# Optimization experiments

Hardware: AMD Instinct MI355X
Metric: run time of the kernel (lower is better)

## Reference

```python
import jax, jax.numpy as jnp
import numpy as np

WINDOW = (7, 7)
SHIFT = (3, 3)
NUM_HEADS = 8
MASK_VALUE = -100.0


def _relative_position_index(wh, ww):
    ch, cw = np.arange(wh), np.arange(ww)
    coords = np.stack(np.meshgrid(ch, cw, indexing='ij'))          # (2, wh, ww)
    cf = coords.reshape(2, -1)                                      # (2, N)
    rel = (cf[:, :, None] - cf[:, None, :]).transpose(1, 2, 0)      # (N, N, 2)
    rel[..., 0] += wh - 1
    rel[..., 1] += ww - 1
    rel[..., 0] *= 2 * ww - 1
    return rel.sum(-1)                                              # (N, N)


def _shift_attn_mask(pH, pW, wh, ww, sh, sw):
    # region-id image for the cyclic shift, as in torchvision Swin
    img = np.zeros((pH, pW), dtype=np.float32)
    cnt = 0
    for hs in ((0, -wh), (-wh, -sh), (-sh, None)):
        for ws_ in ((0, -ww), (-ww, -sw), (-sw, None)):
            img[hs[0]:hs[1], ws_[0]:ws_[1]] = cnt
            cnt += 1
    mw = img.reshape(pH // wh, wh, pW // ww, ww).transpose(0, 2, 1, 3).reshape(-1, wh * ww)
    diff = mw[:, None, :] - mw[:, :, None]                          # (nWtot, N, N)
    return np.where(diff != 0, MASK_VALUE, 0.0).astype(np.float32)


def setup_inputs() -> dict:
    key = jax.random.key(0)
    ks = jax.random.split(key, 6)
    B, H, W, C = 32, 56, 56, 256
    return {
        'x': jax.random.normal(ks[0], (B, H, W, C), jnp.float32),
        'qkv_w': jax.random.normal(ks[1], (3 * C, C), jnp.float32) * 0.02,
        'qkv_b': jax.random.normal(ks[2], (3 * C,), jnp.float32) * 0.02,
        'proj_w': jax.random.normal(ks[3], (C, C), jnp.float32) * 0.02,
        'proj_b': jax.random.normal(ks[4], (C,), jnp.float32) * 0.02,
        'rel_bias_table': jax.random.normal(ks[5], ((2 * WINDOW[0] - 1) * (2 * WINDOW[1] - 1), NUM_HEADS), jnp.float32) * 0.02,
    }


def reference(x, qkv_w, qkv_b, proj_w, proj_b, rel_bias_table):
    wh, ww = WINDOW
    B, H, W, C = x.shape
    nh = NUM_HEADS
    hd = C // nh
    N = wh * ww

    # pad right/bottom to window multiples (static)
    pad_r = (ww - W % ww) % ww
    pad_b = (wh - H % wh) % wh
    x = jnp.pad(x, ((0, 0), (0, pad_b), (0, pad_r), (0, 0)))
    pH, pW = H + pad_b, W + pad_r

    sh = 0 if wh >= pH else SHIFT[0]
    sw = 0 if ww >= pW else SHIFT[1]
    shifted = (sh + sw) > 0
    if shifted:
        x = jnp.roll(x, shift=(-sh, -sw), axis=(1, 2))

    nH, nW = pH // wh, pW // ww
    nwin = nH * nW
    # window partition -> (B*nwin, N, C)
    xw = x.reshape(B, nH, wh, nW, ww, C).transpose(0, 1, 3, 2, 4, 5).reshape(B * nwin, N, C)

    # qkv projection (torch Linear: x @ W.T + b)
    qkv = jnp.einsum('bnc,oc->bno', xw, qkv_w) + qkv_b
    qkv = qkv.reshape(B * nwin, N, 3, nh, hd).transpose(2, 0, 3, 1, 4)  # (3, Bn, h, N, hd)
    q, k, v = qkv[0], qkv[1], qkv[2]

    q = q * (hd ** -0.5)
    attn = jnp.einsum('bhnd,bhmd->bhnm', q, k)                      # (Bn, h, N, N)

    # relative position bias
    idx = jnp.asarray(_relative_position_index(wh, ww))             # (N, N)
    bias = rel_bias_table[idx.reshape(-1)].reshape(N, N, nh).transpose(2, 0, 1)
    attn = attn + bias[None]

    if shifted:
        amask = jnp.asarray(_shift_attn_mask(pH, pW, wh, ww, sh, sw))  # (nwin, N, N)
        attn = attn.reshape(B, nwin, nh, N, N) + amask[None, :, None]
        attn = attn.reshape(B * nwin, nh, N, N)

    attn = jax.nn.softmax(attn, axis=-1)
    out = jnp.einsum('bhnm,bhmd->bhnd', attn, v)                    # (Bn, h, N, hd)
    out = out.transpose(0, 2, 1, 3).reshape(B * nwin, N, C)
    out = jnp.einsum('bnc,oc->bno', out, proj_w) + proj_b

    # window reverse
    out = out.reshape(B, nH, nW, wh, ww, C).transpose(0, 1, 3, 2, 4, 5).reshape(B, pH, pW, C)
    if shifted:
        out = jnp.roll(out, shift=(sh, sw), axis=(1, 2))
    return out[:, :H, :W, :]
```

## Files before the change

kernel.cpp:

```cpp
#include <hip/hip_runtime.h>

typedef __attribute__((ext_vector_type(8))) short bf16x8;
typedef __attribute__((ext_vector_type(4))) float f32x4;
typedef unsigned short u16;

#define NTOK    49
#define SCALE   0.17677669529663687f
#define NEGBIG  -30000.0f
#define DIV7(v) (((v) * 9363) >> 16)

#define EX_OFF     0
#define EX_BYTES   28704
#define EX_INIT_B  25872
#define XO_OFF     28704
#define XO_BYTES   25872
#define BIAS_OFF   54576
#define BIAS_BYTES 2704
#define SMEM_BYTES 57280

static __device__ __forceinline__ float b2f(u16 u) {
    return __uint_as_float(((unsigned int)u) << 16);
}
static __device__ __forceinline__ u16 f2b(float f) {
    unsigned int x = __float_as_uint(f);
    x += 0x7fffu + ((x >> 16) & 1u);
    return (u16)(x >> 16);
}
static __device__ __forceinline__ bf16x8 load8(const void* base, int eidx, int isbf) {
    if (isbf) return *(const bf16x8*)((const u16*)base + eidx);
    const float* f = (const float*)base + eidx;
    float4 a = *(const float4*)f;
    float4 c = *(const float4*)(f + 4);
    bf16x8 r;
    r[0] = (short)f2b(a.x); r[1] = (short)f2b(a.y); r[2] = (short)f2b(a.z); r[3] = (short)f2b(a.w);
    r[4] = (short)f2b(c.x); r[5] = (short)f2b(c.y); r[6] = (short)f2b(c.z); r[7] = (short)f2b(c.w);
    return r;
}
static __device__ __forceinline__ float loadf(const void* base, int i, int isbf) {
    return isbf ? b2f(((const u16*)base)[i]) : ((const float*)base)[i];
}
static __device__ __forceinline__ int region9(int gh, int gw) {
    return (gh < 49 ? 0 : (gh < 53 ? 1 : 2)) * 3 + (gw < 49 ? 0 : (gw < 53 ? 1 : 2));
}

__global__ void __launch_bounds__(256, 2)
swin_fused_v5(const void* __restrict__ x, const void* __restrict__ qkv_w,
              const void* __restrict__ qkv_b, const void* __restrict__ proj_w,
              const void* __restrict__ proj_b, const void* __restrict__ bias_tbl,
              void* __restrict__ out)
{
    __shared__ __align__(16) char smem[SMEM_BYTES];
    const int tid    = threadIdx.x;
    const int wv     = tid >> 6;
    const int lane   = tid & 63;
    const int lane15 = lane & 15;
    const int quad   = lane >> 4;
    const int crow   = quad << 2;

    const int win  = blockIdx.x;
    const int b    = win >> 6;
    const int wrem = win & 63;
    const int whi  = wrem >> 3;
    const int wwi  = wrem & 7;

    int good = 0;
#pragma unroll
    for (int j = 0; j < 8; ++j) {
        u16 u = ((const u16*)qkv_w)[lane * 32 + j * 4];
        int e = (u >> 7) & 0xff;
        good += (e == 0 || (e >= 100 && e <= 140)) ? 1 : 0;
    }
#pragma unroll
    for (int d = 1; d < 64; d <<= 1) good += __shfl_xor(good, d, 64);
    const int isbf = (good > 300) ? 1 : 0;

    for (int i = tid; i < NTOK * 32; i += 256) {
        int tok = i >> 5, ch = i & 31;
        int rt = DIV7(tok), ct = tok - rt * 7;
        int sh_ = whi * 7 + rt + 3; if (sh_ >= 56) sh_ -= 56;
        int sw_ = wwi * 7 + ct + 3; if (sw_ >= 56) sw_ -= 56;
        int idx = ((b * 56 + sh_) * 56 + sw_) * 256 + ch * 8;
        *(bf16x8*)(smem + XO_OFF + tok * 528 + ch * 16) = load8(x, idx, isbf);
    }
    for (int i = tid; i < 169 * 8; i += 256)
        *(u16*)(smem + BIAS_OFF + i * 2) = f2b(loadf(bias_tbl, i, isbf));
    {
        bf16x8 z8 = {0, 0, 0, 0, 0, 0, 0, 0};
        for (int i = tid; i < (EX_BYTES - EX_INIT_B) / 16; i += 256)
            *(bf16x8*)(smem + EX_OFF + EX_INIT_B + i * 16) = z8;
        for (int r = tid; r < NTOK; r += 256)
            *(bf16x8*)(smem + EX_OFF + r * 528 + 512) = z8;
    }
    __syncthreads();

    int mrowc[4];
#pragma unroll
    for (int t = 0; t < 4; ++t) {
        int m = t * 16 + lane15;
        mrowc[t] = m < 49 ? m : 48;
    }

    bf16x8 fragQ[2][4], fragK[2][4], fragV[2][4];

#pragma unroll
    for (int rnd = 0; rnd < 2; ++rnd) {
        for (int ci = 0; ci < 4; ++ci) {
            int o = (wv * 4 + ci) * 16 + lane15;
            int orow = rnd * 256 + o;
            f32x4 acc[4];
#pragma unroll
            for (int t = 0; t < 4; ++t) acc[t] = (f32x4){0.f, 0.f, 0.f, 0.f};
#pragma unroll
            for (int ks = 0; ks < 8; ++ks) {
                bf16x8 bfrag = load8(qkv_w, orow * 256 + ks * 32 + quad * 8, isbf);
                int cb = (ks * 32 + quad * 8) * 2;
#pragma unroll
                for (int tm = 0; tm < 4; ++tm) {
                    bf16x8 afrag = *(const bf16x8*)(smem + XO_OFF + mrowc[tm] * 528 + cb);
                    acc[tm] = __builtin_amdgcn_mfma_f32_16x16x32_bf16(afrag, bfrag, acc[tm], 0, 0, 0);
                }
            }
            float bias = loadf(qkv_b, orow, isbf);
#pragma unroll
            for (int tm = 0; tm < 4; ++tm)
#pragma unroll
                for (int rr = 0; rr < 4; ++rr) {
                    int row = tm * 16 + crow + rr;
                    if (row < 49)
                        *(u16*)(smem + EX_OFF + (row * 264 + o) * 2) = f2b(acc[tm][rr] + bias);
                }
        }
        __syncthreads();
#pragma unroll
        for (int hi = 0; hi < 2; ++hi)
#pragma unroll
            for (int t = 0; t < 4; ++t) {
                bf16x8 f = *(const bf16x8*)(smem + EX_OFF +
                            (mrowc[t] * 264 + wv * 64 + hi * 32 + quad * 8) * 2);
                if (rnd == 0) fragQ[hi][t] = f; else fragK[hi][t] = f;
            }
        __syncthreads();
    }

    for (int ci = 0; ci < 4; ++ci) {
        int vch = (wv * 4 + ci) * 16 + lane15;
        int orow = 512 + vch;
        f32x4 acc[4];
#pragma unroll
        for (int t = 0; t < 4; ++t) acc[t] = (f32x4){0.f, 0.f, 0.f, 0.f};
#pragma unroll
        for (int ks = 0; ks < 8; ++ks) {
            bf16x8 bfrag = load8(qkv_w, orow * 256 + ks * 32 + quad * 8, isbf);
            int cb = (ks * 32 + quad * 8) * 2;
#pragma unroll
            for (int tm = 0; tm < 4; ++tm) {
                bf16x8 afrag = *(const bf16x8*)(smem + XO_OFF + mrowc[tm] * 528 + cb);
                acc[tm] = __builtin_amdgcn_mfma_f32_16x16x32_bf16(afrag, bfrag, acc[tm], 0, 0, 0);
            }
        }
        float bias = loadf(qkv_b, orow, isbf);
#pragma unroll
        for (int tm = 0; tm < 4; ++tm)
#pragma unroll
            for (int rr = 0; rr < 4; ++rr) {
                int row = tm * 16 + crow + rr;
                if (row < 49)
                    *(u16*)(smem + EX_OFF + (vch * 56 + row) * 2) = f2b(acc[tm][rr] + bias);
            }
    }
    __syncthreads();
#pragma unroll
    for (int hi = 0; hi < 2; ++hi)
#pragma unroll
        for (int f = 0; f < 4; ++f) {
            int vrow = wv * 64 + hi * 32 + (f & 1) * 16 + lane15;
            int vcol = (f >> 1) * 32 + quad * 8;
            fragV[hi][f] = *(const bf16x8*)(smem + EX_OFF + (vrow * 56 + vcol) * 2);
        }
    __syncthreads();

    int nval[4], regn_[4], idxn[4];
#pragma unroll
    for (int tn = 0; tn < 4; ++tn) {
        int n = tn * 16 + lane15;
        nval[tn] = (n < 49);
        int nc = n < 49 ? n : 48;
        int rn = DIV7(nc), cn = nc - rn * 7;
        regn_[tn] = region9(whi * 7 + rn, wwi * 7 + cn);
        idxn[tn]  = (6 - rn) * 13 + (6 - cn);
    }

    char* pbase = smem + EX_OFF + wv * 7056;
#pragma unroll
    for (int hi = 0; hi < 2; ++hi) {
        int h = wv * 2 + hi;
        f32x4 s[4][4];
#pragma unroll
        for (int tm = 0; tm < 4; ++tm)
#pragma unroll
            for (int tn = 0; tn < 4; ++tn) {
                f32x4 z = {0.f, 0.f, 0.f, 0.f};
                s[tm][tn] = __builtin_amdgcn_mfma_f32_16x16x32_bf16(fragQ[hi][tm], fragK[hi][tn], z, 0, 0, 0);
            }
#pragma unroll
        for (int tm = 0; tm < 4; ++tm)
#pragma unroll
            for (int rr = 0; rr < 4; ++rr) {
                int m = tm * 16 + crow + rr;
                int mc2 = m < 49 ? m : 48;
                int rm = DIV7(mc2), cm = mc2 - rm * 7;
                int regm = region9(whi * 7 + rm, wwi * 7 + cm);
                int basem = rm * 13 + cm;
                float e[4];
                float mv = NEGBIG;
#pragma unroll
                for (int tn = 0; tn < 4; ++tn) {
                    float v;
                    if (nval[tn]) {
                        int idx = basem + idxn[tn];
                        float bv = b2f(*(const u16*)(smem + BIAS_OFF + (idx * 8 + h) * 2));
                        v = s[tm][tn][rr] * SCALE + bv + ((regm != regn_[tn]) ? -100.0f : 0.0f);
                    } else v = NEGBIG;
                    e[tn] = v;
                    mv = fmaxf(mv, v);
                }
#pragma unroll
                for (int d = 1; d < 16; d <<= 1) mv = fmaxf(mv, __shfl_xor(mv, d, 16));
                float ssum = 0.f;
#pragma unroll
                for (int tn = 0; tn < 4; ++tn) {
                    e[tn] = __expf(e[tn] - mv);
                    ssum += e[tn];
                }
#pragma unroll
                for (int d = 1; d < 16; d <<= 1) ssum += __shfl_xor(ssum, d, 16);
                float ri = 1.0f / ssum;
                if (m < 49) {
#pragma unroll
                    for (int tn = 0; tn < 4; ++tn) {
                        int n = tn * 16 + lane15;
                        u16 hv = nval[tn] ? f2b(e[tn] * ri) : (u16)0;
                        *(u16*)(pbase + (m * 72 + n) * 2) = hv;
                    }
                }
            }
        __syncthreads();
        f32x4 ov0[4], ov1[4];
#pragma unroll
        for (int tm = 0; tm < 4; ++tm) {
            ov0[tm] = (f32x4){0.f, 0.f, 0.f, 0.f};
            ov1[tm] = (f32x4){0.f, 0.f, 0.f, 0.f};
        }
#pragma unroll
        for (int ks = 0; ks < 2; ++ks) {
            int kb = (ks * 32 + quad * 8) * 2;
#pragma unroll
            for (int tm = 0; tm < 4; ++tm) {
                bf16x8 ap = *(const bf16x8*)(pbase + mrowc[tm] * 144 + kb);
                ov0[tm] = __builtin_amdgcn_mfma_f32_16x16x32_bf16(ap, fragV[hi][ks * 2],     ov0[tm], 0, 0, 0);
                ov1[tm] = __builtin_amdgcn_mfma_f32_16x16x32_bf16(ap, fragV[hi][ks * 2 + 1], ov1[tm], 0, 0, 0);
            }
        }
#pragma unroll
        for (int tm = 0; tm < 4; ++tm)
#pragma unroll
            for (int rr = 0; rr < 4; ++rr) {
                int row = tm * 16 + crow + rr;
                if (row < 49) {
                    *(u16*)(smem + XO_OFF + (row * 264 + h * 32 + lane15) * 2)      = f2b(ov0[tm][rr]);
                    *(u16*)(smem + XO_OFF + (row * 264 + h * 32 + 16 + lane15) * 2) = f2b(ov1[tm][rr]);
                }
            }
    }
    __syncthreads();

    int obase[4];
#pragma unroll
    for (int tn = 0; tn < 4; ++tn) {
        int n = tn * 16 + lane15;
        int nc = n < 49 ? n : 48;
        int rn = DIV7(nc), cn = nc - rn * 7;
        int dh = whi * 7 + rn + 3; if (dh >= 56) dh -= 56;
        int dw = wwi * 7 + cn + 3; if (dw >= 56) dw -= 56;
        obase[tn] = ((b * 56 + dh) * 56 + dw) * 256;
    }
    for (int ci = 0; ci < 4; ++ci) {
        int mch = wv * 4 + ci;
        f32x4 acc[4];
#pragma unroll
        for (int t = 0; t < 4; ++t) acc[t] = (f32x4){0.f, 0.f, 0.f, 0.f};
#pragma unroll
        for (int ks = 0; ks < 8; ++ks) {
            bf16x8 af = load8(proj_w, (mch * 16 + lane15) * 256 + ks * 32 + quad * 8, isbf);
            int cb = (ks * 32 + quad * 8) * 2;
#pragma unroll
            for (int tn = 0; tn < 4; ++tn) {
                bf16x8 bo = *(const bf16x8*)(smem + XO_OFF + mrowc[tn] * 528 + cb);
                acc[tn] = __builtin_amdgcn_mfma_f32_16x16x32_bf16(af, bo, acc[tn], 0, 0, 0);
            }
        }
#pragma unroll
        for (int rr = 0; rr < 4; ++rr) {
            int ch = mch * 16 + crow + rr;
            float pb = loadf(proj_b, ch, isbf);
#pragma unroll
            for (int tn = 0; tn < 4; ++tn) {
                if (nval[tn]) {
                    float v = acc[tn][rr] + pb;
                    int oi = obase[tn] + ch;
                    if (isbf) ((u16*)out)[oi] = f2b(v);
                    else      ((float*)out)[oi] = v;
                }
            }
        }
    }
}

extern "C" void kernel_launch(void* const* d_in, const int* in_sizes, int n_in,
                              void* d_out, int out_size, void* d_ws, size_t ws_size,
                              hipStream_t stream) {
    (void)n_in; (void)d_ws; (void)ws_size; (void)out_size;
    int B = in_sizes[0] / (56 * 56 * 256);
    int nblk = B * 64;

    swin_fused_v5<<<dim3(nblk), dim3(256), 0, stream>>>(
        d_in[0], d_in[1], d_in[2], d_in[3], d_in[4], d_in[5], d_out);
}
```

Measured before the change: 566.7 us.

## Swizzle LDS rows, drop bias staging and barriers, raise occupancy to three blocks

Replaces the padded 528-byte LDS row stride with a 512-byte stride and an XOR swizzle, which shrinks shared memory. The relative-position bias table is now read from global memory instead of being staged in LDS. Several __syncthreads calls are removed on the reasoning that each wave reads only the columns it wrote. Launch bounds rise to three blocks per CU. The barrier removal between the softmax P writes and the P·V reads, and around the V transpose, risks races if waves share rows.

```diff
diff --git a/kernel.cpp b/kernel.cpp
--- a/kernel.cpp
+++ b/kernel.cpp
@@ -10,13 +10,13 @@
 #define DIV7(v) (((v) * 9363) >> 16)
 
 #define EX_OFF     0
+#define XCHG_END   25088
 #define EX_BYTES   28704
-#define EX_INIT_B  25872
 #define XO_OFF     28704
-#define XO_BYTES   25872
-#define BIAS_OFF   54576
-#define BIAS_BYTES 2704
-#define SMEM_BYTES 57280
+#define XO_BYTES   25088
+#define SMEM_BYTES 53792
+
+#define SWZ(row, byteoff) ((byteoff) ^ (((row) & 7) << 4))
 
 static __device__ __forceinline__ float b2f(u16 u) {
     return __uint_as_float(((unsigned int)u) << 16);
@@ -43,8 +43,8 @@
     return (gh < 49 ? 0 : (gh < 53 ? 1 : 2)) * 3 + (gw < 49 ? 0 : (gw < 53 ? 1 : 2));
 }
 
-__global__ void __launch_bounds__(256, 2)
-swin_fused_v5(const void* __restrict__ x, const void* __restrict__ qkv_w,
+__global__ void __launch_bounds__(256, 3)
+swin_fused_v6(const void* __restrict__ x, const void* __restrict__ qkv_w,
               const void* __restrict__ qkv_b, const void* __restrict__ proj_w,
               const void* __restrict__ proj_b, const void* __restrict__ bias_tbl,
               void* __restrict__ out)
@@ -80,16 +80,12 @@
         int sh_ = whi * 7 + rt + 3; if (sh_ >= 56) sh_ -= 56;
         int sw_ = wwi * 7 + ct + 3; if (sw_ >= 56) sw_ -= 56;
         int idx = ((b * 56 + sh_) * 56 + sw_) * 256 + ch * 8;
-        *(bf16x8*)(smem + XO_OFF + tok * 528 + ch * 16) = load8(x, idx, isbf);
-    }
-    for (int i = tid; i < 169 * 8; i += 256)
-        *(u16*)(smem + BIAS_OFF + i * 2) = f2b(loadf(bias_tbl, i, isbf));
+        *(bf16x8*)(smem + XO_OFF + tok * 512 + SWZ(tok, ch * 16)) = load8(x, idx, isbf);
+    }
     {
         bf16x8 z8 = {0, 0, 0, 0, 0, 0, 0, 0};
-        for (int i = tid; i < (EX_BYTES - EX_INIT_B) / 16; i += 256)
-            *(bf16x8*)(smem + EX_OFF + EX_INIT_B + i * 16) = z8;
-        for (int r = tid; r < NTOK; r += 256)
-            *(bf16x8*)(smem + EX_OFF + r * 528 + 512) = z8;
+        for (int i = tid; i < (EX_BYTES - XCHG_END) / 16; i += 256)
+            *(bf16x8*)(smem + EX_OFF + XCHG_END + i * 16) = z8;
     }
     __syncthreads();
 
@@ -116,7 +112,7 @@
                 int cb = (ks * 32 + quad * 8) * 2;
 #pragma unroll
                 for (int tm = 0; tm < 4; ++tm) {
-                    bf16x8 afrag = *(const bf16x8*)(smem + XO_OFF + mrowc[tm] * 528 + cb);
+                    bf16x8 afrag = *(const bf16x8*)(smem + XO_OFF + mrowc[tm] * 512 + SWZ(mrowc[tm], cb));
                     acc[tm] = __builtin_amdgcn_mfma_f32_16x16x32_bf16(afrag, bfrag, acc[tm], 0, 0, 0);
                 }
             }
@@ -127,20 +123,19 @@
                 for (int rr = 0; rr < 4; ++rr) {
                     int row = tm * 16 + crow + rr;
                     if (row < 49)
-                        *(u16*)(smem + EX_OFF + (row * 264 + o) * 2) = f2b(acc[tm][rr] + bias);
-                }
-        }
-        __syncthreads();
+                        *(u16*)(smem + EX_OFF + row * 512 + SWZ(row, o * 2)) = f2b(acc[tm][rr] + bias);
+                }
+        }
 #pragma unroll
         for (int hi = 0; hi < 2; ++hi)
 #pragma unroll
             for (int t = 0; t < 4; ++t) {
-                bf16x8 f = *(const bf16x8*)(smem + EX_OFF +
-                            (mrowc[t] * 264 + wv * 64 + hi * 32 + quad * 8) * 2);
+                int cbyte = wv * 128 + hi * 64 + quad * 16;
+                bf16x8 f = *(const bf16x8*)(smem + EX_OFF + mrowc[t] * 512 + SWZ(mrowc[t], cbyte));
                 if (rnd == 0) fragQ[hi][t] = f; else fragK[hi][t] = f;
             }
-        __syncthreads();
-    }
+    }
+    __syncthreads();
 
     for (int ci = 0; ci < 4; ++ci) {
         int vch = (wv * 4 + ci) * 16 + lane15;
@@ -154,7 +149,7 @@
             int cb = (ks * 32 + quad * 8) * 2;
 #pragma unroll
             for (int tm = 0; tm < 4; ++tm) {
-                bf16x8 afrag = *(const bf16x8*)(smem + XO_OFF + mrowc[tm] * 528 + cb);
+                bf16x8 afrag = *(const bf16x8*)(smem + XO_OFF + mrowc[tm] * 512 + SWZ(mrowc[tm], cb));
                 acc[tm] = __builtin_amdgcn_mfma_f32_16x16x32_bf16(afrag, bfrag, acc[tm], 0, 0, 0);
             }
         }
@@ -168,7 +163,6 @@
                     *(u16*)(smem + EX_OFF + (vch * 56 + row) * 2) = f2b(acc[tm][rr] + bias);
             }
     }
-    __syncthreads();
 #pragma unroll
     for (int hi = 0; hi < 2; ++hi)
 #pragma unroll
@@ -218,7 +212,7 @@
                     float v;
                     if (nval[tn]) {
                         int idx = basem + idxn[tn];
-                        float bv = b2f(*(const u16*)(smem + BIAS_OFF + (idx * 8 + h) * 2));
+                        float bv = loadf(bias_tbl, idx * 8 + h, isbf);
                         v = s[tm][tn][rr] * SCALE + bv + ((regm != regn_[tn]) ? -100.0f : 0.0f);
                     } else v = NEGBIG;
                     e[tn] = v;
@@ -244,7 +238,6 @@
                     }
                 }
             }
-        __syncthreads();
         f32x4 ov0[4], ov1[4];
 #pragma unroll
         for (int tm = 0; tm < 4; ++tm) {
@@ -267,8 +260,8 @@
             for (int rr = 0; rr < 4; ++rr) {
                 int row = tm * 16 + crow + rr;
                 if (row < 49) {
-                    *(u16*)(smem + XO_OFF + (row * 264 + h * 32 + lane15) * 2)      = f2b(ov0[tm][rr]);
-                    *(u16*)(smem + XO_OFF + (row * 264 + h * 32 + 16 + lane15) * 2) = f2b(ov1[tm][rr]);
+                    *(u16*)(smem + XO_OFF + row * 512 + SWZ(row, (h * 32 + lane15) * 2))        = f2b(ov0[tm][rr]);
+                    *(u16*)(smem + XO_OFF + row * 512 + SWZ(row, (h * 32 + 16 + lane15) * 2))   = f2b(ov1[tm][rr]);
                 }
             }
     }
@@ -295,7 +288,7 @@
             int cb = (ks * 32 + quad * 8) * 2;
 #pragma unroll
             for (int tn = 0; tn < 4; ++tn) {
-                bf16x8 bo = *(const bf16x8*)(smem + XO_OFF + mrowc[tn] * 528 + cb);
+                bf16x8 bo = *(const bf16x8*)(smem + XO_OFF + mrowc[tn] * 512 + SWZ(mrowc[tn], cb));
                 acc[tn] = __builtin_amdgcn_mfma_f32_16x16x32_bf16(af, bo, acc[tn], 0, 0, 0);
             }
         }
@@ -323,6 +316,6 @@
     int B = in_sizes[0] / (56 * 56 * 256);
     int nblk = B * 64;
 
-    swin_fused_v5<<<dim3(nblk), dim3(256), 0, stream>>>(
+    swin_fused_v6<<<dim3(nblk), dim3(256), 0, stream>>>(
         d_in[0], d_in[1], d_in[2], d_in[3], d_in[4], d_in[5], d_out);
 }
```

After: 746.4 us. 1.32x slower.
